# Optimization experiments

Measured on AMD Instinct MI355X. Metric: run time of the kernel, lower is better.

The kernel has to match this reference:

```python
import jax, jax.numpy as jnp
import numpy as np

DEPTH, HEADS, DH, BUCKET, NHASH = 4, 8, 64, 64, 4
DIM, VOCAB, BATCH, SEQ = 512, 50000, 2, 2048
LN_EPS = 1e-5
SELF_ATTN_VAL = -5e4  # TOKEN_SELF_ATTN_VALUE in reformer_pytorch


def layer_norm(x, s, b):
    mu = x.mean(-1, keepdims=True)
    var = ((x - mu) ** 2).mean(-1, keepdims=True)
    return (x - mu) / jnp.sqrt(var + LN_EPS) * s + b


def sincos(t, dh):
    # FixedPositionalEmbedding: emb = cat(sin, cos) of t x dh/2 angles
    inv = 1.0 / (10000.0 ** (jnp.arange(0, dh, 2, dtype=jnp.float32) / dh))
    ang = jnp.arange(t, dtype=jnp.float32)[:, None] * inv[None, :]
    return jnp.sin(ang), jnp.cos(ang)


def apply_rotary(qk, sin, cos):
    # qk: [B*H, T, DH]; sin/cos: [T, DH/2]; interleaved-pair rotary as in reformer_pytorch
    sin2 = jnp.repeat(sin, 2, axis=-1)[None]
    cos2 = jnp.repeat(cos, 2, axis=-1)[None]
    xr = qk.reshape(qk.shape[0], qk.shape[1], -1, 2)
    rot = jnp.stack((-xr[..., 1], xr[..., 0]), axis=-1).reshape(qk.shape)
    return qk * cos2 + rot * sin2


def lsh_attention(qk, v, rot):
    # qk, v: [B, T, dh] (B = batch*heads, shared-QK); rot: [dh, NHASH, n_buckets//2]
    B, T, dh = qk.shape
    nb = T // BUCKET
    rv = jnp.einsum('btf,fhi->bhti', qk, rot)           # [B, NHASH, T, nb/2]
    rv = jnp.concatenate([rv, -rv], axis=-1)
    buckets = jnp.argmax(rv, axis=-1)                    # [B, NHASH, T]
    buckets = (buckets + (jnp.arange(NHASH) * nb)[None, :, None]).reshape(B, NHASH * T)
    ticker = jnp.arange(NHASH * T) % T
    key = T * buckets + ticker[None, :]                  # unique sort keys
    sticker = jnp.argsort(key, axis=-1)                  # [B, NHASH*T]
    undo = jnp.argsort(sticker, axis=-1)
    st = sticker % T
    sqk = jnp.take_along_axis(qk, st[:, :, None], axis=1)
    sv = jnp.take_along_axis(v, st[:, :, None], axis=1)
    C = NHASH * nb                                       # num chunks, each BUCKET long
    bq_t = st.reshape(B, C, BUCKET)
    bq = sqk.reshape(B, C, BUCKET, dh)
    bv = sv.reshape(B, C, BUCKET, dh)
    bk = bq / jnp.maximum(jnp.linalg.norm(bq, axis=-1, keepdims=True), 1e-12)

    def look_one_back(a):
        return jnp.concatenate([a, jnp.roll(a, 1, axis=1)], axis=2)

    bk, bv, bkv_t = look_one_back(bk), look_one_back(bv), look_one_back(bq_t)
    dots = jnp.einsum('bcie,bcje->bcij', bq, bk) * (dh ** -0.5)
    dots = jnp.where(bq_t[:, :, :, None] == bkv_t[:, :, None, :], SELF_ATTN_VAL, dots)
    lse = jax.nn.logsumexp(dots, axis=-1, keepdims=True)
    p = jnp.exp(dots - lse)
    bo = jnp.einsum('bcij,bcje->bcie', p, bv)
    so = bo.reshape(B, NHASH * T, dh)
    slog = lse.reshape(B, NHASH * T)
    o = jnp.take_along_axis(so, undo[:, :, None], axis=1).reshape(B, NHASH, T, dh)
    lg = jnp.take_along_axis(slog, undo, axis=1).reshape(B, NHASH, T, 1)
    w = jnp.exp(lg - jax.nn.logsumexp(lg, axis=1, keepdims=True))
    return jnp.sum(o * w, axis=1)                        # [B, T, dh]


def attn_block(x, s, bln, Wqk, Wv, Wo, bo, rot, sin, cos):
    b, t, _ = x.shape
    xn = layer_norm(x, s, bln)
    qk = (xn @ Wqk).reshape(b, t, HEADS, DH).transpose(0, 2, 1, 3).reshape(b * HEADS, t, DH)
    v = (xn @ Wv).reshape(b, t, HEADS, DH).transpose(0, 2, 1, 3).reshape(b * HEADS, t, DH)
    qk = apply_rotary(qk, sin, cos)
    o = lsh_attention(qk, v, rot)
    o = o.reshape(b, HEADS, t, DH).transpose(0, 2, 1, 3).reshape(b, t, HEADS * DH)
    return o @ Wo + bo


def ff_block(x, s, b, W1, b1, W2, b2):
    xn = layer_norm(x, s, b)
    return jax.nn.gelu(xn @ W1 + b1, approximate=False) @ W2 + b2


def reference(x, token_emb, ln1_s, ln1_b, Wqk, Wv, Wo, bo, ln2_s, ln2_b, W1, b1, W2, b2, rotations, lnf_s, lnf_b, Wf1, bf1, Wout, bout):
    e = token_emb[x]                                     # [B, T, DIM]
    sin, cos = sincos(x.shape[1], DH)
    x1 = x2 = e                                          # reversible twin streams
    for i in range(DEPTH):
        x1 = x1 + attn_block(x2, ln1_s[i], ln1_b[i], Wqk[i], Wv[i], Wo[i], bo[i], rotations[i], sin, cos)
        x2 = x2 + ff_block(x1, ln2_s[i], ln2_b[i], W1[i], b1[i], W2[i], b2[i])
    h = layer_norm((x1 + x2) * 0.5, lnf_s, lnf_b)
    h = h.mean(axis=1)
    h = jax.nn.relu(h @ Wf1 + bf1)
    return h @ Wout + bout


def setup_inputs():
    key = jax.random.key(0)
    ks = jax.random.split(key, 10)
    nb = SEQ // BUCKET
    s = 0.02
    return {
        'x': jax.random.randint(ks[0], (BATCH, SEQ), 0, VOCAB),
        'token_emb': jax.random.normal(ks[1], (VOCAB, DIM), jnp.float32) * s,
        'ln1_s': jnp.ones((DEPTH, DIM), jnp.float32),
        'ln1_b': jnp.zeros((DEPTH, DIM), jnp.float32),
        'Wqk': jax.random.normal(ks[2], (DEPTH, DIM, HEADS * DH), jnp.float32) * s,
        'Wv': jax.random.normal(ks[3], (DEPTH, DIM, HEADS * DH), jnp.float32) * s,
        'Wo': jax.random.normal(ks[4], (DEPTH, HEADS * DH, DIM), jnp.float32) * s,
        'bo': jnp.zeros((DEPTH, DIM), jnp.float32),
        'ln2_s': jnp.ones((DEPTH, DIM), jnp.float32),
        'ln2_b': jnp.zeros((DEPTH, DIM), jnp.float32),
        'W1': jax.random.normal(ks[5], (DEPTH, DIM, 4 * DIM), jnp.float32) * s,
        'b1': jnp.zeros((DEPTH, 4 * DIM), jnp.float32),
        'W2': jax.random.normal(ks[6], (DEPTH, 4 * DIM, DIM), jnp.float32) * s,
        'b2': jnp.zeros((DEPTH, DIM), jnp.float32),
        'rotations': jax.random.normal(ks[7], (DEPTH, DH, NHASH, nb // 2), jnp.float32),
        'lnf_s': jnp.ones((DIM,), jnp.float32),
        'lnf_b': jnp.zeros((DIM,), jnp.float32),
        'Wf1': jax.random.normal(ks[8], (DIM, 256), jnp.float32) * s,
        'bf1': jnp.zeros((256,), jnp.float32),
        'Wout': jax.random.normal(ks[9], (256, 1), jnp.float32) * s,
        'bout': jnp.zeros((1,), jnp.float32),
    }
```

## Files before the change

### kernel.cpp

```cpp
#include <hip/hip_runtime.h>
#include <math.h>

#define TSEQ   2048
#define DIMM   512
#define NHEAD  8
#define DHD    64
#define BHD    16
#define NHASHK 4
#define CHUNKS 128
#define FFD    2048
#define NROWS  4096

#define OFF_WQK 0
#define OFF_WV  262144
#define OFF_WO  524288
#define OFF_W1  786432
#define OFF_W2  1835008
#define WT_TOT  2883584

typedef unsigned short u16;
typedef _Float16 f16;
typedef __attribute__((ext_vector_type(8))) _Float16 f16x8;
typedef __attribute__((ext_vector_type(4))) float f32x4;
typedef __attribute__((ext_vector_type(8))) unsigned short ushort8v;
typedef __attribute__((ext_vector_type(4))) unsigned short ushort4v;

__device__ inline u16 h16(float f) {
  union { f16 h; u16 u; } x;
  x.h = (f16)f;
  return x.u;
}
__device__ inline float f16f(u16 u) {
  union { u16 u; f16 h; } x;
  x.u = u;
  return (float)x.h;
}
__device__ inline f16x8 mk8f(unsigned a, unsigned b, unsigned c, unsigned d) {
  union { unsigned u[4]; f16x8 v; } x;
  x.u[0] = a; x.u[1] = b; x.u[2] = c; x.u[3] = d;
  return x.v;
}
__device__ inline float gelu_exact(float v) {
  return 0.5f * v * (1.0f + erff(v * 0.70710678118654752f));
}
__device__ inline int swz128(int row, int colbyte) {
  return row * 128 + (colbyte ^ ((row & 7) << 4));
}

__global__ __launch_bounds__(128) void k_embed(const int* __restrict__ x, const float* __restrict__ emb,
                                               float* __restrict__ x1, float* __restrict__ x2) {
  int row = blockIdx.x;
  int tok = x[row];
  float4 v = ((const float4*)(emb + (size_t)tok * DIMM))[threadIdx.x];
  ((float4*)(x1 + (size_t)row * DIMM))[threadIdx.x] = v;
  ((float4*)(x2 + (size_t)row * DIMM))[threadIdx.x] = v;
}

__global__ __launch_bounds__(256) void k_sincos(float* __restrict__ sin_t, float* __restrict__ cos_t) {
  int idx = blockIdx.x * 256 + threadIdx.x;
  int t = idx >> 5, i = idx & 31;
  float inv = powf(10000.0f, -(float)(2 * i) / 64.0f);
  float ang = (float)t * inv;
  sin_t[idx] = sinf(ang);
  cos_t[idx] = cosf(ang);
}

__global__ __launch_bounds__(256) void k_layernorm(const float* __restrict__ x, const float* __restrict__ g,
                                                   const float* __restrict__ b, u16* __restrict__ dst) {
  int row = blockIdx.x, tid = threadIdx.x;
  const float* xr = x + (size_t)row * DIMM;
  float v0 = xr[tid], v1 = xr[tid + 256];
  int lane = tid & 63, w = tid >> 6;
  __shared__ float red[8];
  float s = v0 + v1;
#pragma unroll
  for (int o = 32; o; o >>= 1) s += __shfl_xor(s, o);
  if (lane == 0) red[w] = s;
  __syncthreads();
  float mu = (red[0] + red[1] + red[2] + red[3]) * (1.0f / DIMM);
  float d0 = v0 - mu, d1 = v1 - mu;
  float q = d0 * d0 + d1 * d1;
#pragma unroll
  for (int o = 32; o; o >>= 1) q += __shfl_xor(q, o);
  if (lane == 0) red[4 + w] = q;
  __syncthreads();
  float var = (red[4] + red[5] + red[6] + red[7]) * (1.0f / DIMM);
  float rstd = 1.0f / sqrtf(var + 1e-5f);
  size_t base = (size_t)row * DIMM;
  dst[base + tid] = h16(d0 * rstd * g[tid] + b[tid]);
  dst[base + tid + 256] = h16(d1 * rstd * g[tid + 256] + b[tid + 256]);
}

__global__ __launch_bounds__(256) void k_prep(const float* __restrict__ Wqk, const float* __restrict__ Wv,
                                              const float* __restrict__ Wo, const float* __restrict__ W1,
                                              const float* __restrict__ W2, const float* __restrict__ rot,
                                              u16* __restrict__ wt16, u16* __restrict__ rt16) {
  __shared__ float tile[32][33];
  const int idx = blockIdx.x;
  const float* src;
  u16* dh;
  int K, N, k0, n0;
  if (idx < 768) {
    int w = idx >> 8, r = idx & 255;
    K = 512; N = 512; k0 = (r >> 4) << 5; n0 = (r & 15) << 5;
    src = (w == 0) ? Wqk : (w == 1) ? Wv : Wo;
    dh = wt16 + (size_t)w * 262144;
  } else if (idx < 1792) {
    int r = idx - 768;
    K = 512; N = 2048; k0 = (r >> 6) << 5; n0 = (r & 63) << 5;
    src = W1; dh = wt16 + OFF_W1;
  } else if (idx < 2816) {
    int r = idx - 1792;
    K = 2048; N = 512; k0 = (r >> 4) << 5; n0 = (r & 15) << 5;
    src = W2; dh = wt16 + OFF_W2;
  } else {
    int r = idx - 2816;
    K = 64; N = 64; k0 = (r >> 1) << 5; n0 = (r & 1) << 5;
    src = rot; dh = rt16;
  }
  const int t = threadIdx.x;
  const int r = t >> 3, c4 = (t & 7) << 2;
  float4 v = *(const float4*)&src[(size_t)(k0 + r) * N + n0 + c4];
  tile[r][c4] = v.x; tile[r][c4 + 1] = v.y; tile[r][c4 + 2] = v.z; tile[r][c4 + 3] = v.w;
  __syncthreads();
  u16 hs[4];
#pragma unroll
  for (int i = 0; i < 4; ++i) hs[i] = h16(tile[c4 + i][r]);
  size_t o = (size_t)(n0 + r) * K + k0 + c4;
  *(ushort4v*)&dh[o] = (ushort4v){hs[0], hs[1], hs[2], hs[3]};
}

template <int BM, int STORE>
__global__ __launch_bounds__(256) void k_gemm16(
    const u16* __restrict__ A, const u16* __restrict__ Bt,
    const float* __restrict__ bias, float* __restrict__ out,
    u16* __restrict__ out16, u16* __restrict__ qk16, u16* __restrict__ v16,
    int K, int N,
    const float* __restrict__ sin_t, const float* __restrict__ cos_t) {
  constexpr int MF = BM / 32;
  constexpr int ACH = BM / 32;
  __shared__ __align__(16) char AsB[BM * 128];
  __shared__ __align__(16) char BsB[64 * 128];
  const int bm = blockIdx.x * BM, bn = blockIdx.y << 6;
  const int tid = threadIdx.x, lane = tid & 63, wid = tid >> 6;
  const int wm = (wid >> 1) * (BM / 2), wn = (wid & 1) << 5;
  const int l16 = lane & 15, g = lane >> 4;
  f32x4 acc[MF][2];
#pragma unroll
  for (int m = 0; m < MF; ++m) { acc[m][0] = (f32x4){0,0,0,0}; acc[m][1] = (f32x4){0,0,0,0}; }

  const int srow = tid >> 3;
  const int scolb = (tid & 7) << 4;
  const u16* ap = A + (size_t)(bm + srow) * K + ((tid & 7) << 3);
  const u16* bp = Bt + (size_t)(bn + srow) * K + ((tid & 7) << 3);

  ushort8v pa[ACH], pb[2];
#pragma unroll
  for (int i = 0; i < ACH; ++i) pa[i] = *(const ushort8v*)(ap + (size_t)(i << 5) * K);
#pragma unroll
  for (int i = 0; i < 2; ++i) pb[i] = *(const ushort8v*)(bp + (size_t)(i << 5) * K);

  for (int k0 = 0;;) {
#pragma unroll
    for (int i = 0; i < ACH; ++i)
      *(ushort8v*)(AsB + swz128(srow + (i << 5), scolb)) = pa[i];
#pragma unroll
    for (int i = 0; i < 2; ++i)
      *(ushort8v*)(BsB + swz128(srow + (i << 5), scolb)) = pb[i];
    __syncthreads();
    const int kn = k0 + 64;
    if (kn < K) {
#pragma unroll
      for (int i = 0; i < ACH; ++i) pa[i] = *(const ushort8v*)(ap + (size_t)(i << 5) * K + kn);
#pragma unroll
      for (int i = 0; i < 2; ++i) pb[i] = *(const ushort8v*)(bp + (size_t)(i << 5) * K + kn);
    }
    f16x8 af[MF][2], bf[2][2];
#pragma unroll
    for (int m = 0; m < MF; ++m)
#pragma unroll
      for (int ks = 0; ks < 2; ++ks)
        af[m][ks] = *(const f16x8*)(AsB + swz128(wm + (m << 4) + l16, ((ks << 2) + g) << 4));
#pragma unroll
    for (int n = 0; n < 2; ++n)
#pragma unroll
      for (int ks = 0; ks < 2; ++ks)
        bf[n][ks] = *(const f16x8*)(BsB + swz128(wn + (n << 4) + l16, ((ks << 2) + g) << 4));
#pragma unroll
    for (int m = 0; m < MF; ++m)
#pragma unroll
      for (int n = 0; n < 2; ++n)
#pragma unroll
        for (int ks = 0; ks < 2; ++ks)
          acc[m][n] = __builtin_amdgcn_mfma_f32_16x16x32_f16(af[m][ks], bf[n][ks], acc[m][n], 0, 0, 0);
    if (kn >= K) break;
    __syncthreads();
    k0 = kn;
  }
#pragma unroll
  for (int m = 0; m < MF; ++m) {
#pragma unroll
    for (int n = 0; n < 2; ++n) {
      const int gn = bn + wn + (n << 4) + l16;
      float bv = 0.f;
      if (STORE == 1 || STORE == 4) bv = bias[gn];
#pragma unroll
      for (int r = 0; r < 4; ++r) {
        const int gm = bm + wm + (m << 4) + (g << 2) + r;
        float val = acc[m][n][r];
        if (STORE == 1) {
          out[(size_t)gm * N + gn] += val + bv;
        } else if (STORE == 4) {
          out16[(size_t)gm * N + gn] = h16(gelu_exact(val + bv));
        } else {
          const float pv = __shfl_xor(val, 1);
          const int bb = gm >> 11, tt = gm & (TSEQ - 1);
          if (gn < 512) {
            const int hh = gn >> 6, dd = gn & 63;
            const int ip = dd >> 1;
            float cz = cos_t[tt * 32 + ip], sz = sin_t[tt * 32 + ip];
            float o = (dd & 1) ? (val * cz + pv * sz) : (val * cz - pv * sz);
            qk16[((size_t)((bb * NHEAD + hh) * TSEQ + tt)) * DHD + dd] = h16(o);
          } else {
            const int gnn = gn - 512;
            const int hh = gnn >> 6, dd = gnn & 63;
            v16[((size_t)((bb * NHEAD + hh) * TSEQ + tt)) * DHD + dd] = h16(val);
          }
        }
      }
    }
  }
}

__global__ __launch_bounds__(256) void k_bucket_gemm(const u16* __restrict__ qk16,
                                                     const u16* __restrict__ rt16,
                                                     int* __restrict__ bucket) {
  __shared__ __align__(16) u16 Ah[128][72];
  __shared__ __align__(16) u16 Bh[64][72];
  const int bm = blockIdx.x << 7;
  const int tid = threadIdx.x, lane = tid & 63, wid = tid >> 6;
  const int l16 = lane & 15, g = lane >> 4;
  {
    const int r = tid >> 1, hf = tid & 1;
    const u16* src = qk16 + (size_t)(bm + r) * 64 + hf * 32;
#pragma unroll
    for (int i = 0; i < 4; ++i)
      *(ushort8v*)&Ah[r][hf * 32 + i * 8] = *(const ushort8v*)(src + i * 8);
  }
  if (tid < 128) {
    const int r = tid >> 1, hf = tid & 1;
    const u16* src = rt16 + (size_t)r * 64 + hf * 32;
#pragma unroll
    for (int i = 0; i < 4; ++i)
      *(ushort8v*)&Bh[r][hf * 32 + i * 8] = *(const ushort8v*)(src + i * 8);
  }
  __syncthreads();
  const int wm = (wid >> 1) << 6, wn = (wid & 1) << 5;
  f32x4 acc[4][2];
#pragma unroll
  for (int m = 0; m < 4; ++m) { acc[m][0] = (f32x4){0,0,0,0}; acc[m][1] = (f32x4){0,0,0,0}; }
#pragma unroll
  for (int s = 0; s < 2; ++s) {
    f16x8 bfr[2];
#pragma unroll
    for (int n = 0; n < 2; ++n)
      bfr[n] = *(const f16x8*)&Bh[wn + (n << 4) + l16][s * 32 + g * 8];
#pragma unroll
    for (int m = 0; m < 4; ++m) {
      f16x8 afr = *(const f16x8*)&Ah[wm + (m << 4) + l16][s * 32 + g * 8];
#pragma unroll
      for (int n = 0; n < 2; ++n)
        acc[m][n] = __builtin_amdgcn_mfma_f32_16x16x32_f16(afr, bfr[n], acc[m][n], 0, 0, 0);
    }
  }
#pragma unroll
  for (int m = 0; m < 4; ++m)
#pragma unroll
    for (int n = 0; n < 2; ++n) {
      const int hcol = (wn >> 4) + n;
#pragma unroll
      for (int r = 0; r < 4; ++r) {
        float v = acc[m][n][r];
        float best = v; int bi = l16;
        if (-v > best) { best = -v; bi = 16 + l16; }
#pragma unroll
        for (int o = 1; o < 16; o <<= 1) {
          float ob = __shfl_xor(best, o);
          int obi = __shfl_xor(bi, o);
          if (ob > best || (ob == best && obi < bi)) { best = ob; bi = obi; }
        }
        if (l16 == 0) {
          int gm = bm + wm + (m << 4) + (g << 2) + r;
          int bh_ = gm >> 11, t = gm & (TSEQ - 1);
          bucket[((size_t)(bh_ * NHASHK) + hcol) * TSEQ + t] = bi;
        }
      }
    }
}

__global__ __launch_bounds__(256) void k_sort(const int* __restrict__ bucket, int* __restrict__ st) {
  __shared__ int hist[256][33];
  __shared__ int bbase[32];
  const int seg = blockIdx.x;
  const int tid = threadIdx.x;
  const int* bk = bucket + (size_t)seg * TSEQ;
  int4 u0 = *(const int4*)(bk + tid * 8);
  int4 u1 = *(const int4*)(bk + tid * 8 + 4);
  int myb[8] = {u0.x, u0.y, u0.z, u0.w, u1.x, u1.y, u1.z, u1.w};
#pragma unroll
  for (int j = 0; j < 33; ++j) hist[tid][j] = 0;
  __syncthreads();
#pragma unroll
  for (int i = 0; i < 8; ++i) hist[tid][myb[i]]++;
  __syncthreads();
  if (tid < 32) {
    int run = 0;
    for (int gq = 0; gq < 256; ++gq) { int c = hist[gq][tid]; hist[gq][tid] = run; run += c; }
    bbase[tid] = run;
  }
  __syncthreads();
  if (tid == 0) {
    int s = 0;
    for (int j = 0; j < 32; ++j) { int c = bbase[j]; bbase[j] = s; s += c; }
  }
  __syncthreads();
  int* dst = st + (size_t)seg * TSEQ;
#pragma unroll
  for (int i = 0; i < 8; ++i) {
    int b = myb[i];
    int p = bbase[b] + hist[tid][b];
    hist[tid][b]++;
    dst[p] = tid * 8 + i;
  }
}

__global__ __launch_bounds__(256) void k_attn(const u16* __restrict__ qk16,
                                              const u16* __restrict__ v16,
                                              const int* __restrict__ st,
                                              float* __restrict__ o4, float* __restrict__ lg) {
  __shared__ __align__(16) char Kb[128 * 128];
  __shared__ float inv_norm[128];
  __shared__ int tids[128];
  __shared__ float pn[256];
  const int blk = blockIdx.x;
  const int c = blk & (CHUNKS - 1), bh = blk >> 7;
  const int h = c >> 5;
  const int tid = threadIdx.x, lane = tid & 63, wid = tid >> 6;
  const int l16 = lane & 15, g = lane >> 4;

  if (tid < 128) {
    int cc = (tid < 64) ? c : ((c + CHUNKS - 1) & (CHUNKS - 1));
    tids[tid] = st[bh * (NHASHK * TSEQ) + cc * 64 + (tid & 63)];
  }
  __syncthreads();
  {
    const int r = tid >> 1, hf = tid & 1;
    const u16* src = qk16 + ((size_t)bh * TSEQ + tids[r]) * 64 + hf * 32;
    float ss = 0.f;
#pragma unroll
    for (int i = 0; i < 4; ++i) {
      ushort8v u = *(const ushort8v*)(src + i * 8);
      *(ushort8v*)(Kb + swz128(r, hf * 64 + i * 16)) = u;
#pragma unroll
      for (int j = 0; j < 8; ++j) { float f = f16f(u[j]); ss += f * f; }
    }
    pn[tid] = ss;
  }
  __syncthreads();
  if (tid < 128) {
    float s2 = pn[2 * tid] + pn[2 * tid + 1];
    inv_norm[tid] = 1.0f / fmaxf(sqrtf(s2), 1e-12f);
  }
  __syncthreads();

  const int qrow = (wid << 4) + l16;
  const int tq = tids[qrow];
  const size_t obase = (size_t)(bh * NHASHK + h) * TSEQ + tq;

  f32x4 accs[8];
#pragma unroll
  for (int i = 0; i < 8; ++i) accs[i] = (f32x4){0, 0, 0, 0};
#pragma unroll
  for (int s = 0; s < 2; ++s) {
    f16x8 qf = *(const f16x8*)(Kb + swz128(qrow, ((s << 2) + g) << 4));
#pragma unroll
    for (int mf = 0; mf < 8; ++mf) {
      f16x8 afr = *(const f16x8*)(Kb + swz128(mf * 16 + l16, ((s << 2) + g) << 4));
      accs[mf] = __builtin_amdgcn_mfma_f32_16x16x32_f16(afr, qf, accs[mf], 0, 0, 0);
    }
  }
  float pv[8][4];
  float mx = -3e38f;
#pragma unroll
  for (int mf = 0; mf < 8; ++mf) {
    float4 invn = *(const float4*)&inv_norm[mf * 16 + g * 4];
    int4 tk = *(const int4*)&tids[mf * 16 + g * 4];
    float inva[4] = {invn.x, invn.y, invn.z, invn.w};
    int tka[4] = {tk.x, tk.y, tk.z, tk.w};
#pragma unroll
    for (int r = 0; r < 4; ++r) {
      float d = accs[mf][r] * inva[r] * 0.125f;
      if (tka[r] == tq) d = -5e4f;
      pv[mf][r] = d;
      mx = fmaxf(mx, d);
    }
  }
  mx = fmaxf(mx, __shfl_xor(mx, 16));
  mx = fmaxf(mx, __shfl_xor(mx, 32));
  float sum = 0.f;
#pragma unroll
  for (int mf = 0; mf < 8; ++mf)
#pragma unroll
    for (int r = 0; r < 4; ++r) {
      float e = __expf(pv[mf][r] - mx);
      pv[mf][r] = e;
      sum += e;
    }
  sum += __shfl_xor(sum, 16);
  sum += __shfl_xor(sum, 32);
  float lse = __logf(sum) + mx;
  float rs = 1.0f / sum;
  if (g == 0) lg[obase] = lse;
  unsigned P2[8][2];
#pragma unroll
  for (int mf = 0; mf < 8; ++mf)
#pragma unroll
    for (int m = 0; m < 2; ++m) {
      float p0 = pv[mf][2 * m] * rs, p1 = pv[mf][2 * m + 1] * rs;
      P2[mf][m] = (unsigned)h16(p0) | ((unsigned)h16(p1) << 16);
    }
  f32x4 acco[4];
#pragma unroll
  for (int i = 0; i < 4; ++i) acco[i] = (f32x4){0, 0, 0, 0};
  const u16* vbase = v16 + (size_t)bh * TSEQ * 64;
#pragma unroll
  for (int s = 0; s < 4; ++s) {
    unsigned bw[4];
#pragma unroll
    for (int w = 0; w < 4; ++w) {
      int srl = l16 + (((2 * g + (w >> 1)) & 3) << 4);
      unsigned a0 = __shfl(P2[2 * s][w & 1], srl);
      unsigned a1 = __shfl(P2[2 * s + 1][w & 1], srl);
      bw[w] = (g >> 1) ? a1 : a0;
    }
    f16x8 pb = mk8f(bw[0], bw[1], bw[2], bw[3]);
    int4 t0 = *(const int4*)&tids[s * 32 + g * 8];
    int4 t1 = *(const int4*)&tids[s * 32 + g * 8 + 4];
    int ro[8] = {t0.x, t0.y, t0.z, t0.w, t1.x, t1.y, t1.z, t1.w};
#pragma unroll
    for (int mf = 0; mf < 4; ++mf) {
      const int dcol = mf * 16 + l16;
      u16 vw[8];
#pragma unroll
      for (int j = 0; j < 8; ++j) vw[j] = vbase[(size_t)ro[j] * 64 + dcol];
      f16x8 vf = mk8f((unsigned)vw[0] | ((unsigned)vw[1] << 16),
                      (unsigned)vw[2] | ((unsigned)vw[3] << 16),
                      (unsigned)vw[4] | ((unsigned)vw[5] << 16),
                      (unsigned)vw[6] | ((unsigned)vw[7] << 16));
      acco[mf] = __builtin_amdgcn_mfma_f32_16x16x32_f16(vf, pb, acco[mf], 0, 0, 0);
    }
  }
#pragma unroll
  for (int mf = 0; mf < 4; ++mf)
    *(float4*)&o4[obase * 64 + mf * 16 + g * 4] =
        make_float4(acco[mf][0], acco[mf][1], acco[mf][2], acco[mf][3]);
}

__global__ __launch_bounds__(256) void k_combine(const float* __restrict__ o4, const float* __restrict__ lg,
                                                 u16* __restrict__ ctx16) {
  int tok = blockIdx.x * 4 + (threadIdx.x >> 6);
  int dd = threadIdx.x & 63;
  int bh = tok >> 11, t = tok & (TSEQ - 1);
  size_t base = (size_t)bh * NHASHK * TSEQ + t;
  float l0 = lg[base], l1 = lg[base + TSEQ], l2 = lg[base + 2 * TSEQ], l3 = lg[base + 3 * TSEQ];
  float m = fmaxf(fmaxf(l0, l1), fmaxf(l2, l3));
  float e0 = expf(l0 - m), e1 = expf(l1 - m), e2 = expf(l2 - m), e3 = expf(l3 - m);
  float inv = 1.0f / (e0 + e1 + e2 + e3);
  float o = (e0 * o4[base * 64 + dd] + e1 * o4[(base + TSEQ) * 64 + dd] +
             e2 * o4[(base + 2 * TSEQ) * 64 + dd] + e3 * o4[(base + 3 * TSEQ) * 64 + dd]) * inv;
  int b = bh >> 3, hh = bh & 7;
  ctx16[((size_t)(b * TSEQ + t)) * DIMM + hh * DHD + dd] = h16(o);
}

__global__ __launch_bounds__(256) void k_final_stats(const float* __restrict__ x1, const float* __restrict__ x2,
                                                     float2* __restrict__ stats) {
  int row = blockIdx.x, tid = threadIdx.x;
  const float* p1 = x1 + (size_t)row * DIMM;
  const float* p2 = x2 + (size_t)row * DIMM;
  float v0 = 0.5f * (p1[tid] + p2[tid]);
  float v1 = 0.5f * (p1[tid + 256] + p2[tid + 256]);
  int lane = tid & 63, w = tid >> 6;
  __shared__ float red[8];
  float s = v0 + v1;
#pragma unroll
  for (int o = 32; o; o >>= 1) s += __shfl_xor(s, o);
  if (lane == 0) red[w] = s;
  __syncthreads();
  float mu = (red[0] + red[1] + red[2] + red[3]) * (1.0f / DIMM);
  float d0 = v0 - mu, d1 = v1 - mu;
  float q = d0 * d0 + d1 * d1;
#pragma unroll
  for (int o = 32; o; o >>= 1) q += __shfl_xor(q, o);
  if (lane == 0) red[4 + w] = q;
  __syncthreads();
  if (tid == 0) {
    float var = (red[4] + red[5] + red[6] + red[7]) * (1.0f / DIMM);
    stats[row] = make_float2(mu, 1.0f / sqrtf(var + 1e-5f));
  }
}

__global__ __launch_bounds__(256) void k_colmean1(const float* __restrict__ x1, const float* __restrict__ x2,
                                                  const float2* __restrict__ stats, float* __restrict__ part) {
  int blk = blockIdx.x;
  int bb = blk >> 5, ch = blk & 31;
  int d = threadIdx.x;
  float a0 = 0.f, a1 = 0.f;
  for (int i = 0; i < 64; ++i) {
    int row = bb * TSEQ + (ch << 6) + i;
    float2 sr = stats[row];
    size_t base = (size_t)row * DIMM;
    a0 += (0.5f * (x1[base + d] + x2[base + d]) - sr.x) * sr.y;
    a1 += (0.5f * (x1[base + d + 256] + x2[base + d + 256]) - sr.x) * sr.y;
  }
  part[(size_t)blk * DIMM + d] = a0;
  part[(size_t)blk * DIMM + d + 256] = a1;
}

__global__ __launch_bounds__(256) void k_colmean2(const float* __restrict__ part,
                                                  const float* __restrict__ g, const float* __restrict__ b,
                                                  float* __restrict__ hm) {
  int idx = blockIdx.x * 256 + threadIdx.x;
  int bb = idx >> 9, d = idx & 511;
  float s = 0.f;
  for (int c = 0; c < 32; ++c) s += part[(size_t)(bb * 32 + c) * DIMM + d];
  hm[idx] = s * (1.0f / TSEQ) * g[d] + b[d];
}

__global__ __launch_bounds__(256) void k_head1(const float* __restrict__ hm, const float* __restrict__ Wf1,
                                               const float* __restrict__ bf1, float* __restrict__ r1) {
  int b = blockIdx.x, j = threadIdx.x;
  float acc = 0;
  for (int k = 0; k < DIMM; ++k) acc += hm[b * DIMM + k] * Wf1[k * 256 + j];
  r1[b * 256 + j] = fmaxf(acc + bf1[j], 0.0f);
}

__global__ __launch_bounds__(256) void k_head2(const float* __restrict__ r1, const float* __restrict__ Wout,
                                               const float* __restrict__ bout, float* __restrict__ outp) {
  int b = blockIdx.x;
  int tid = threadIdx.x, lane = tid & 63, w = tid >> 6;
  float v = r1[b * 256 + tid] * Wout[tid];
#pragma unroll
  for (int o = 32; o; o >>= 1) v += __shfl_xor(v, o);
  __shared__ float red[4];
  if (lane == 0) red[w] = v;
  __syncthreads();
  if (tid == 0) outp[b] = red[0] + red[1] + red[2] + red[3] + bout[0];
}

extern "C" void kernel_launch(void* const* d_in, const int* in_sizes, int n_in,
                              void* d_out, int out_size, void* d_ws, size_t ws_size,
                              hipStream_t stream) {
  const int*   x         = (const int*)d_in[0];
  const float* token_emb = (const float*)d_in[1];
  const float* ln1_s     = (const float*)d_in[2];
  const float* ln1_b     = (const float*)d_in[3];
  const float* Wqk       = (const float*)d_in[4];
  const float* Wv        = (const float*)d_in[5];
  const float* Wo        = (const float*)d_in[6];
  const float* bo        = (const float*)d_in[7];
  const float* ln2_s     = (const float*)d_in[8];
  const float* ln2_b     = (const float*)d_in[9];
  const float* W1        = (const float*)d_in[10];
  const float* b1        = (const float*)d_in[11];
  const float* W2        = (const float*)d_in[12];
  const float* b2        = (const float*)d_in[13];
  const float* rotations = (const float*)d_in[14];
  const float* lnf_s     = (const float*)d_in[15];
  const float* lnf_b     = (const float*)d_in[16];
  const float* Wf1       = (const float*)d_in[17];
  const float* bf1       = (const float*)d_in[18];
  const float* Wout      = (const float*)d_in[19];
  const float* bout      = (const float*)d_in[20];
  float* out = (float*)d_out;

  char* ws = (char*)d_ws;
  size_t off = 0;
  auto alloc = [&](size_t nbytes) {
    char* p = ws + off;
    off += (nbytes + 255) & ~(size_t)255;
    return p;
  };
  float*  x1     = (float*)alloc((size_t)NROWS * DIMM * 4);
  float*  x2     = (float*)alloc((size_t)NROWS * DIMM * 4);
  u16*    xn16   = (u16*)alloc((size_t)NROWS * DIMM * 2);
  u16*    qk16   = (u16*)alloc((size_t)BHD * TSEQ * DHD * 2);
  u16*    v16    = (u16*)alloc((size_t)BHD * TSEQ * DHD * 2);
  u16*    ffh16  = (u16*)alloc((size_t)NROWS * FFD * 2);
  float*  o4     = (float*)alloc((size_t)BHD * NHASHK * TSEQ * DHD * 4);
  float*  lg     = (float*)alloc((size_t)BHD * NHASHK * TSEQ * 4);
  float*  sin_t  = (float*)alloc((size_t)TSEQ * 32 * 4);
  float*  cos_t  = (float*)alloc((size_t)TSEQ * 32 * 4);
  float2* stats  = (float2*)alloc((size_t)NROWS * 8);
  float*  part   = (float*)alloc((size_t)64 * DIMM * 4);
  float*  hm     = (float*)alloc(2 * DIMM * 4);
  float*  r1     = (float*)alloc(2 * 256 * 4);
  int*    bucket = (int*)alloc((size_t)BHD * NHASHK * TSEQ * 4);
  int*    st     = (int*)alloc((size_t)BHD * NHASHK * TSEQ * 4);
  u16*    wt16   = (u16*)alloc((size_t)WT_TOT * 2);
  u16*    rott16 = (u16*)alloc(64 * 64 * 2);
  u16*    ctx16  = xn16;

  k_embed<<<NROWS, 128, 0, stream>>>(x, token_emb, x1, x2);
  k_sincos<<<(TSEQ * 32) / 256, 256, 0, stream>>>(sin_t, cos_t);

  for (int L = 0; L < 4; ++L) {
    const float* wqk = Wqk + (size_t)L * DIMM * DIMM;
    const float* wv  = Wv  + (size_t)L * DIMM * DIMM;
    const float* wo  = Wo  + (size_t)L * DIMM * DIMM;
    const float* w1  = W1  + (size_t)L * DIMM * FFD;
    const float* w2  = W2  + (size_t)L * FFD * DIMM;
    const float* rot = rotations + (size_t)L * DHD * NHASHK * 16;

    k_prep<<<2820, 256, 0, stream>>>(wqk, wv, wo, w1, w2, rot, wt16, rott16);
    k_layernorm<<<NROWS, 256, 0, stream>>>(x2, ln1_s + L * DIMM, ln1_b + L * DIMM, xn16);
    k_gemm16<128, 5><<<dim3(32, 16), 256, 0, stream>>>(
        xn16, wt16 + OFF_WQK, nullptr, nullptr, nullptr, qk16, v16, 512, 1024, sin_t, cos_t);
    k_bucket_gemm<<<BHD * TSEQ / 128, 256, 0, stream>>>(qk16, rott16, bucket);
    k_sort<<<BHD * NHASHK, 256, 0, stream>>>(bucket, st);
    k_attn<<<BHD * CHUNKS, 256, 0, stream>>>(qk16, v16, st, o4, lg);
    k_combine<<<(BHD * TSEQ) / 4, 256, 0, stream>>>(o4, lg, ctx16);
    k_gemm16<64, 1><<<dim3(64, 8), 256, 0, stream>>>(
        ctx16, wt16 + OFF_WO, bo + L * DIMM, x1, nullptr, nullptr, nullptr, 512, 512, nullptr, nullptr);
    k_layernorm<<<NROWS, 256, 0, stream>>>(x1, ln2_s + L * DIMM, ln2_b + L * DIMM, xn16);
    k_gemm16<128, 4><<<dim3(32, 32), 256, 0, stream>>>(
        xn16, wt16 + OFF_W1, b1 + L * FFD, nullptr, ffh16, nullptr, nullptr, 512, 2048, nullptr, nullptr);
    k_gemm16<64, 1><<<dim3(64, 8), 256, 0, stream>>>(
        ffh16, wt16 + OFF_W2, b2 + L * DIMM, x2, nullptr, nullptr, nullptr, 2048, 512, nullptr, nullptr);
  }

  k_final_stats<<<NROWS, 256, 0, stream>>>(x1, x2, stats);
  k_colmean1<<<64, 256, 0, stream>>>(x1, x2, stats, part);
  k_colmean2<<<4, 256, 0, stream>>>(part, lnf_s, lnf_b, hm);
  k_head1<<<2, 256, 0, stream>>>(hm, Wf1, bf1, r1);
  k_head2<<<2, 256, 0, stream>>>(r1, Wout, bout, out);
}
```

Measured before the change: 611.5 us.

## Batch weight prep, double-buffer GEMM prefetch, stage V in LDS, parallelize final head

Several independent changes. Weight conversion for all four layers now runs in one launch before the layer loop instead of once per layer. The GEMM main loop gets a two-stage register prefetch so global loads run two k-steps ahead. The attention kernel stages V transposed into padded LDS in place of scattered global gathers. The final-stats, column-mean and head kernels are fused or split to expose more parallelism. The costs are more workspace for the converted weights, more registers in the GEMM, extra LDS in attention, and a GEMM loop that assumes an even number of k-steps.

```diff
diff --git a/kernel.cpp b/kernel.cpp
--- a/kernel.cpp
+++ b/kernel.cpp
@@ -46,6 +46,7 @@
 __device__ inline int swz128(int row, int colbyte) {
   return row * 128 + (colbyte ^ ((row & 7) << 4));
 }
+#define VT(d, k) ((d) * 264 + (((d) & 32) ? 8 : 0) + ((k) << 1))
 
 __global__ __launch_bounds__(128) void k_embed(const int* __restrict__ x, const float* __restrict__ emb,
                                                float* __restrict__ x1, float* __restrict__ x2) {
@@ -96,7 +97,16 @@
                                               const float* __restrict__ W2, const float* __restrict__ rot,
                                               u16* __restrict__ wt16, u16* __restrict__ rt16) {
   __shared__ float tile[32][33];
-  const int idx = blockIdx.x;
+  const int L = blockIdx.x / 2820;
+  const int idx = blockIdx.x - L * 2820;
+  Wqk += (size_t)L * 262144;
+  Wv  += (size_t)L * 262144;
+  Wo  += (size_t)L * 262144;
+  W1  += (size_t)L * 1048576;
+  W2  += (size_t)L * 1048576;
+  rot += (size_t)L * 4096;
+  u16* wt = wt16 + (size_t)L * WT_TOT;
+  u16* rt = rt16 + (size_t)L * 4096;
   const float* src;
   u16* dh;
   int K, N, k0, n0;
@@ -104,19 +114,19 @@
     int w = idx >> 8, r = idx & 255;
     K = 512; N = 512; k0 = (r >> 4) << 5; n0 = (r & 15) << 5;
     src = (w == 0) ? Wqk : (w == 1) ? Wv : Wo;
-    dh = wt16 + (size_t)w * 262144;
+    dh = wt + (size_t)w * 262144;
   } else if (idx < 1792) {
     int r = idx - 768;
     K = 512; N = 2048; k0 = (r >> 6) << 5; n0 = (r & 63) << 5;
-    src = W1; dh = wt16 + OFF_W1;
+    src = W1; dh = wt + OFF_W1;
   } else if (idx < 2816) {
     int r = idx - 1792;
     K = 2048; N = 512; k0 = (r >> 4) << 5; n0 = (r & 15) << 5;
-    src = W2; dh = wt16 + OFF_W2;
+    src = W2; dh = wt + OFF_W2;
   } else {
     int r = idx - 2816;
     K = 64; N = 64; k0 = (r >> 1) << 5; n0 = (r & 1) << 5;
-    src = rot; dh = rt16;
+    src = rot; dh = rt;
   }
   const int t = threadIdx.x;
   const int r = t >> 3, c4 = (t & 7) << 2;
@@ -154,28 +164,32 @@
   const u16* ap = A + (size_t)(bm + srow) * K + ((tid & 7) << 3);
   const u16* bp = Bt + (size_t)(bn + srow) * K + ((tid & 7) << 3);
 
-  ushort8v pa[ACH], pb[2];
-#pragma unroll
-  for (int i = 0; i < ACH; ++i) pa[i] = *(const ushort8v*)(ap + (size_t)(i << 5) * K);
-#pragma unroll
-  for (int i = 0; i < 2; ++i) pb[i] = *(const ushort8v*)(bp + (size_t)(i << 5) * K);
-
-  for (int k0 = 0;;) {
+  ushort8v paA[ACH], pbA[2], paB[ACH], pbB[2];
+#pragma unroll
+  for (int i = 0; i < ACH; ++i) paA[i] = *(const ushort8v*)(ap + (size_t)(i << 5) * K);
+#pragma unroll
+  for (int i = 0; i < 2; ++i) pbA[i] = *(const ushort8v*)(bp + (size_t)(i << 5) * K);
+#pragma unroll
+  for (int i = 0; i < ACH; ++i) paB[i] = *(const ushort8v*)(ap + (size_t)(i << 5) * K + 64);
+#pragma unroll
+  for (int i = 0; i < 2; ++i) pbB[i] = *(const ushort8v*)(bp + (size_t)(i << 5) * K + 64);
+
+  auto gstep = [&](ushort8v (&PA)[ACH], ushort8v (&PB)[2], int S) {
 #pragma unroll
     for (int i = 0; i < ACH; ++i)
-      *(ushort8v*)(AsB + swz128(srow + (i << 5), scolb)) = pa[i];
+      *(ushort8v*)(AsB + swz128(srow + (i << 5), scolb)) = PA[i];
 #pragma unroll
     for (int i = 0; i < 2; ++i)
-      *(ushort8v*)(BsB + swz128(srow + (i << 5), scolb)) = pb[i];
+      *(ushort8v*)(BsB + swz128(srow + (i << 5), scolb)) = PB[i];
     __syncthreads();
-    const int kn = k0 + 64;
-    if (kn < K) {
-#pragma unroll
-      for (int i = 0; i < ACH; ++i) pa[i] = *(const ushort8v*)(ap + (size_t)(i << 5) * K + kn);
-#pragma unroll
-      for (int i = 0; i < 2; ++i) pb[i] = *(const ushort8v*)(bp + (size_t)(i << 5) * K + kn);
-    }
-    f16x8 af[MF][2], bf[2][2];
+    const int kf = (S + 2) << 6;
+    if (kf < K) {
+#pragma unroll
+      for (int i = 0; i < ACH; ++i) PA[i] = *(const ushort8v*)(ap + (size_t)(i << 5) * K + kf);
+#pragma unroll
+      for (int i = 0; i < 2; ++i) PB[i] = *(const ushort8v*)(bp + (size_t)(i << 5) * K + kf);
+    }
+    f16x8 af[MF][2], bfr[2][2];
 #pragma unroll
     for (int m = 0; m < MF; ++m)
 #pragma unroll
@@ -185,18 +199,23 @@
     for (int n = 0; n < 2; ++n)
 #pragma unroll
       for (int ks = 0; ks < 2; ++ks)
-        bf[n][ks] = *(const f16x8*)(BsB + swz128(wn + (n << 4) + l16, ((ks << 2) + g) << 4));
+        bfr[n][ks] = *(const f16x8*)(BsB + swz128(wn + (n << 4) + l16, ((ks << 2) + g) << 4));
 #pragma unroll
     for (int m = 0; m < MF; ++m)
 #pragma unroll
       for (int n = 0; n < 2; ++n)
 #pragma unroll
         for (int ks = 0; ks < 2; ++ks)
-          acc[m][n] = __builtin_amdgcn_mfma_f32_16x16x32_f16(af[m][ks], bf[n][ks], acc[m][n], 0, 0, 0);
-    if (kn >= K) break;
+          acc[m][n] = __builtin_amdgcn_mfma_f32_16x16x32_f16(af[m][ks], bfr[n][ks], acc[m][n], 0, 0, 0);
     __syncthreads();
-    k0 = kn;
-  }
+  };
+
+  const int nsteps = K >> 6;
+  for (int s = 0; s < nsteps; s += 2) {
+    gstep(paA, pbA, s);
+    gstep(paB, pbB, s + 1);
+  }
+
 #pragma unroll
   for (int m = 0; m < MF; ++m) {
 #pragma unroll
@@ -339,6 +358,7 @@
                                               const int* __restrict__ st,
                                               float* __restrict__ o4, float* __restrict__ lg) {
   __shared__ __align__(16) char Kb[128 * 128];
+  __shared__ __align__(16) char Vb[64 * 264 + 16];
   __shared__ float inv_norm[128];
   __shared__ int tids[128];
   __shared__ float pn[256];
@@ -355,14 +375,19 @@
   __syncthreads();
   {
     const int r = tid >> 1, hf = tid & 1;
-    const u16* src = qk16 + ((size_t)bh * TSEQ + tids[r]) * 64 + hf * 32;
+    const u16* qsrc = qk16 + ((size_t)bh * TSEQ + tids[r]) * 64 + hf * 32;
+    const u16* vsrc = v16 + ((size_t)bh * TSEQ + tids[r]) * 64 + hf * 32;
     float ss = 0.f;
 #pragma unroll
     for (int i = 0; i < 4; ++i) {
-      ushort8v u = *(const ushort8v*)(src + i * 8);
+      ushort8v u = *(const ushort8v*)(qsrc + i * 8);
       *(ushort8v*)(Kb + swz128(r, hf * 64 + i * 16)) = u;
 #pragma unroll
       for (int j = 0; j < 8; ++j) { float f = f16f(u[j]); ss += f * f; }
+      ushort8v vv8 = *(const ushort8v*)(vsrc + i * 8);
+#pragma unroll
+      for (int j = 0; j < 8; ++j)
+        *(u16*)(Vb + VT(hf * 32 + i * 8 + j, r)) = vv8[j];
     }
     pn[tid] = ss;
   }
@@ -432,7 +457,6 @@
   f32x4 acco[4];
 #pragma unroll
   for (int i = 0; i < 4; ++i) acco[i] = (f32x4){0, 0, 0, 0};
-  const u16* vbase = v16 + (size_t)bh * TSEQ * 64;
 #pragma unroll
   for (int s = 0; s < 4; ++s) {
     unsigned bw[4];
@@ -444,19 +468,13 @@
       bw[w] = (g >> 1) ? a1 : a0;
     }
     f16x8 pb = mk8f(bw[0], bw[1], bw[2], bw[3]);
-    int4 t0 = *(const int4*)&tids[s * 32 + g * 8];
-    int4 t1 = *(const int4*)&tids[s * 32 + g * 8 + 4];
-    int ro[8] = {t0.x, t0.y, t0.z, t0.w, t1.x, t1.y, t1.z, t1.w};
+    const int k0 = s * 32 + g * 8;
 #pragma unroll
     for (int mf = 0; mf < 4; ++mf) {
       const int dcol = mf * 16 + l16;
-      u16 vw[8];
-#pragma unroll
-      for (int j = 0; j < 8; ++j) vw[j] = vbase[(size_t)ro[j] * 64 + dcol];
-      f16x8 vf = mk8f((unsigned)vw[0] | ((unsigned)vw[1] << 16),
-                      (unsigned)vw[2] | ((unsigned)vw[3] << 16),
-                      (unsigned)vw[4] | ((unsigned)vw[5] << 16),
-                      (unsigned)vw[6] | ((unsigned)vw[7] << 16));
+      uint2 v0 = *(const uint2*)(Vb + VT(dcol, k0));
+      uint2 v1 = *(const uint2*)(Vb + VT(dcol, k0 + 4));
+      f16x8 vf = mk8f(v0.x, v0.y, v1.x, v1.y);
       acco[mf] = __builtin_amdgcn_mfma_f32_16x16x32_f16(vf, pb, acco[mf], 0, 0, 0);
     }
   }
@@ -482,73 +500,72 @@
   ctx16[((size_t)(b * TSEQ + t)) * DIMM + hh * DHD + dd] = h16(o);
 }
 
-__global__ __launch_bounds__(256) void k_final_stats(const float* __restrict__ x1, const float* __restrict__ x2,
-                                                     float2* __restrict__ stats) {
-  int row = blockIdx.x, tid = threadIdx.x;
-  const float* p1 = x1 + (size_t)row * DIMM;
-  const float* p2 = x2 + (size_t)row * DIMM;
-  float v0 = 0.5f * (p1[tid] + p2[tid]);
-  float v1 = 0.5f * (p1[tid + 256] + p2[tid + 256]);
-  int lane = tid & 63, w = tid >> 6;
+__global__ __launch_bounds__(256) void k_colmean1(const float* __restrict__ x1, const float* __restrict__ x2,
+                                                  float* __restrict__ part) {
+  const int blk = blockIdx.x;
+  const int bb = blk >> 8, ch = blk & 255;
+  const int tid = threadIdx.x, lane = tid & 63, w = tid >> 6;
   __shared__ float red[8];
-  float s = v0 + v1;
-#pragma unroll
-  for (int o = 32; o; o >>= 1) s += __shfl_xor(s, o);
-  if (lane == 0) red[w] = s;
-  __syncthreads();
-  float mu = (red[0] + red[1] + red[2] + red[3]) * (1.0f / DIMM);
-  float d0 = v0 - mu, d1 = v1 - mu;
-  float q = d0 * d0 + d1 * d1;
-#pragma unroll
-  for (int o = 32; o; o >>= 1) q += __shfl_xor(q, o);
-  if (lane == 0) red[4 + w] = q;
-  __syncthreads();
-  if (tid == 0) {
+  float a0 = 0.f, a1 = 0.f;
+  for (int i = 0; i < 8; ++i) {
+    int row = bb * TSEQ + ch * 8 + i;
+    size_t base = (size_t)row * DIMM;
+    float v0 = 0.5f * (x1[base + tid] + x2[base + tid]);
+    float v1 = 0.5f * (x1[base + tid + 256] + x2[base + tid + 256]);
+    float s = v0 + v1;
+#pragma unroll
+    for (int o = 32; o; o >>= 1) s += __shfl_xor(s, o);
+    if (lane == 0) red[w] = s;
+    __syncthreads();
+    float mu = (red[0] + red[1] + red[2] + red[3]) * (1.0f / DIMM);
+    float d0 = v0 - mu, d1 = v1 - mu;
+    float q = d0 * d0 + d1 * d1;
+#pragma unroll
+    for (int o = 32; o; o >>= 1) q += __shfl_xor(q, o);
+    if (lane == 0) red[4 + w] = q;
+    __syncthreads();
     float var = (red[4] + red[5] + red[6] + red[7]) * (1.0f / DIMM);
-    stats[row] = make_float2(mu, 1.0f / sqrtf(var + 1e-5f));
-  }
-}
-
-__global__ __launch_bounds__(256) void k_colmean1(const float* __restrict__ x1, const float* __restrict__ x2,
-                                                  const float2* __restrict__ stats, float* __restrict__ part) {
-  int blk = blockIdx.x;
-  int bb = blk >> 5, ch = blk & 31;
-  int d = threadIdx.x;
-  float a0 = 0.f, a1 = 0.f;
-  for (int i = 0; i < 64; ++i) {
-    int row = bb * TSEQ + (ch << 6) + i;
-    float2 sr = stats[row];
-    size_t base = (size_t)row * DIMM;
-    a0 += (0.5f * (x1[base + d] + x2[base + d]) - sr.x) * sr.y;
-    a1 += (0.5f * (x1[base + d + 256] + x2[base + d + 256]) - sr.x) * sr.y;
-  }
-  part[(size_t)blk * DIMM + d] = a0;
-  part[(size_t)blk * DIMM + d + 256] = a1;
+    float rstd = 1.0f / sqrtf(var + 1e-5f);
+    a0 += d0 * rstd;
+    a1 += d1 * rstd;
+    __syncthreads();
+  }
+  part[(size_t)blk * DIMM + tid] = a0;
+  part[(size_t)blk * DIMM + tid + 256] = a1;
 }
 
 __global__ __launch_bounds__(256) void k_colmean2(const float* __restrict__ part,
                                                   const float* __restrict__ g, const float* __restrict__ b,
                                                   float* __restrict__ hm) {
-  int idx = blockIdx.x * 256 + threadIdx.x;
-  int bb = idx >> 9, d = idx & 511;
+  int gidx = blockIdx.x * 256 + threadIdx.x;
+  int oid = gidx >> 3, sub = gidx & 7;
+  int bb = oid >> 9, d = oid & 511;
   float s = 0.f;
-  for (int c = 0; c < 32; ++c) s += part[(size_t)(bb * 32 + c) * DIMM + d];
-  hm[idx] = s * (1.0f / TSEQ) * g[d] + b[d];
+  for (int c = sub; c < 256; c += 8) s += part[((size_t)(bb * 256 + c)) * DIMM + d];
+  s += __shfl_xor(s, 1);
+  s += __shfl_xor(s, 2);
+  s += __shfl_xor(s, 4);
+  if (sub == 0) hm[oid] = s * (1.0f / TSEQ) * g[d] + b[d];
 }
 
 __global__ __launch_bounds__(256) void k_head1(const float* __restrict__ hm, const float* __restrict__ Wf1,
-                                               const float* __restrict__ bf1, float* __restrict__ r1) {
-  int b = blockIdx.x, j = threadIdx.x;
+                                               float* __restrict__ r1p) {
+  int b = blockIdx.x & 1, kc = blockIdx.x >> 1;
+  int j = threadIdx.x;
   float acc = 0;
-  for (int k = 0; k < DIMM; ++k) acc += hm[b * DIMM + k] * Wf1[k * 256 + j];
-  r1[b * 256 + j] = fmaxf(acc + bf1[j], 0.0f);
-}
-
-__global__ __launch_bounds__(256) void k_head2(const float* __restrict__ r1, const float* __restrict__ Wout,
-                                               const float* __restrict__ bout, float* __restrict__ outp) {
+  for (int k = kc * 64; k < kc * 64 + 64; ++k) acc += hm[b * DIMM + k] * Wf1[k * 256 + j];
+  r1p[(size_t)(kc * 2 + b) * 256 + j] = acc;
+}
+
+__global__ __launch_bounds__(256) void k_head2(const float* __restrict__ r1p, const float* __restrict__ bf1,
+                                               const float* __restrict__ Wout, const float* __restrict__ bout,
+                                               float* __restrict__ outp) {
   int b = blockIdx.x;
   int tid = threadIdx.x, lane = tid & 63, w = tid >> 6;
-  float v = r1[b * 256 + tid] * Wout[tid];
+  float s = 0.f;
+#pragma unroll
+  for (int kc = 0; kc < 8; ++kc) s += r1p[(size_t)(kc * 2 + b) * 256 + tid];
+  float v = fmaxf(s + bf1[tid], 0.0f) * Wout[tid];
 #pragma unroll
   for (int o = 32; o; o >>= 1) v += __shfl_xor(v, o);
   __shared__ float red[4];
@@ -600,47 +617,41 @@
   float*  lg     = (float*)alloc((size_t)BHD * NHASHK * TSEQ * 4);
   float*  sin_t  = (float*)alloc((size_t)TSEQ * 32 * 4);
   float*  cos_t  = (float*)alloc((size_t)TSEQ * 32 * 4);
-  float2* stats  = (float2*)alloc((size_t)NROWS * 8);
-  float*  part   = (float*)alloc((size_t)64 * DIMM * 4);
+  float*  part   = (float*)alloc((size_t)512 * DIMM * 4);
   float*  hm     = (float*)alloc(2 * DIMM * 4);
-  float*  r1     = (float*)alloc(2 * 256 * 4);
+  float*  r1p    = (float*)alloc(16 * 256 * 4);
   int*    bucket = (int*)alloc((size_t)BHD * NHASHK * TSEQ * 4);
   int*    st     = (int*)alloc((size_t)BHD * NHASHK * TSEQ * 4);
-  u16*    wt16   = (u16*)alloc((size_t)WT_TOT * 2);
-  u16*    rott16 = (u16*)alloc(64 * 64 * 2);
+  u16*    wt16   = (u16*)alloc((size_t)4 * WT_TOT * 2);
+  u16*    rott16 = (u16*)alloc((size_t)4 * 64 * 64 * 2);
   u16*    ctx16  = xn16;
 
   k_embed<<<NROWS, 128, 0, stream>>>(x, token_emb, x1, x2);
   k_sincos<<<(TSEQ * 32) / 256, 256, 0, stream>>>(sin_t, cos_t);
+  k_prep<<<4 * 2820, 256, 0, stream>>>(Wqk, Wv, Wo, W1, W2, rotations, wt16, rott16);
 
   for (int L = 0; L < 4; ++L) {
-    const float* wqk = Wqk + (size_t)L * DIMM * DIMM;
-    const float* wv  = Wv  + (size_t)L * DIMM * DIMM;
-    const float* wo  = Wo  + (size_t)L * DIMM * DIMM;
-    const float* w1  = W1  + (size_t)L * DIMM * FFD;
-    const float* w2  = W2  + (size_t)L * FFD * DIMM;
-    const float* rot = rotations + (size_t)L * DHD * NHASHK * 16;
-
-    k_prep<<<2820, 256, 0, stream>>>(wqk, wv, wo, w1, w2, rot, wt16, rott16);
+    u16* wt = wt16 + (size_t)L * WT_TOT;
+    u16* rt = rott16 + (size_t)L * 4096;
+
     k_layernorm<<<NROWS, 256, 0, stream>>>(x2, ln1_s + L * DIMM, ln1_b + L * DIMM, xn16);
     k_gemm16<128, 5><<<dim3(32, 16), 256, 0, stream>>>(
-        xn16, wt16 + OFF_WQK, nullptr, nullptr, nullptr, qk16, v16, 512, 1024, sin_t, cos_t);
-    k_bucket_gemm<<<BHD * TSEQ / 128, 256, 0, stream>>>(qk16, rott16, bucket);
+        xn16, wt + OFF_WQK, nullptr, nullptr, nullptr, qk16, v16, 512, 1024, sin_t, cos_t);
+    k_bucket_gemm<<<BHD * TSEQ / 128, 256, 0, stream>>>(qk16, rt, bucket);
     k_sort<<<BHD * NHASHK, 256, 0, stream>>>(bucket, st);
     k_attn<<<BHD * CHUNKS, 256, 0, stream>>>(qk16, v16, st, o4, lg);
     k_combine<<<(BHD * TSEQ) / 4, 256, 0, stream>>>(o4, lg, ctx16);
     k_gemm16<64, 1><<<dim3(64, 8), 256, 0, stream>>>(
-        ctx16, wt16 + OFF_WO, bo + L * DIMM, x1, nullptr, nullptr, nullptr, 512, 512, nullptr, nullptr);
+        ctx16, wt + OFF_WO, bo + L * DIMM, x1, nullptr, nullptr, nullptr, 512, 512, nullptr, nullptr);
     k_layernorm<<<NROWS, 256, 0, stream>>>(x1, ln2_s + L * DIMM, ln2_b + L * DIMM, xn16);
     k_gemm16<128, 4><<<dim3(32, 32), 256, 0, stream>>>(
-        xn16, wt16 + OFF_W1, b1 + L * FFD, nullptr, ffh16, nullptr, nullptr, 512, 2048, nullptr, nullptr);
+        xn16, wt + OFF_W1, b1 + L * FFD, nullptr, ffh16, nullptr, nullptr, 512, 2048, nullptr, nullptr);
     k_gemm16<64, 1><<<dim3(64, 8), 256, 0, stream>>>(
-        ffh16, wt16 + OFF_W2, b2 + L * DIMM, x2, nullptr, nullptr, nullptr, 2048, 512, nullptr, nullptr);
-  }
-
-  k_final_stats<<<NROWS, 256, 0, stream>>>(x1, x2, stats);
-  k_colmean1<<<64, 256, 0, stream>>>(x1, x2, stats, part);
-  k_colmean2<<<4, 256, 0, stream>>>(part, lnf_s, lnf_b, hm);
-  k_head1<<<2, 256, 0, stream>>>(hm, Wf1, bf1, r1);
-  k_head2<<<2, 256, 0, stream>>>(r1, Wout, bout, out);
-}
+        ffh16, wt + OFF_W2, b2 + L * DIMM, x2, nullptr, nullptr, nullptr, 2048, 512, nullptr, nullptr);
+  }
+
+  k_colmean1<<<512, 256, 0, stream>>>(x1, x2, part);
+  k_colmean2<<<32, 256, 0, stream>>>(part, lnf_s, lnf_b, hm);
+  k_head1<<<16, 256, 0, stream>>>(hm, Wf1, r1p);
+  k_head2<<<2, 256, 0, stream>>>(r1p, bf1, Wout, bout, out);
+}
```

Result: faster. 570.5 us (-6.7%).
